# Kernel tuning notes

Hardware: AMD Instinct MI355X
Metric: run time of the kernel (lower is better)

The kernel has to match this reference:

```python
import jax, jax.numpy as jnp
import numpy as np

NHEAD = 8

def setup_inputs() -> dict:
    key = jax.random.key(0)
    ks = jax.random.split(key, 7)
    B, N, D = 8, 1024, 512
    scale = 1.0 / np.sqrt(D)
    return {
        "x": jax.random.normal(ks[0], (B, N, D), dtype=jnp.float32),
        "graph_bias": jax.random.normal(ks[1], (B, N, N), dtype=jnp.float32),
        "in_proj_w": jax.random.normal(ks[2], (3 * D, D), dtype=jnp.float32) * scale,
        "in_proj_b": jax.random.normal(ks[3], (3 * D,), dtype=jnp.float32) * 0.02,
        "out_proj_w": jax.random.normal(ks[4], (D, D), dtype=jnp.float32) * scale,
        "out_proj_b": jax.random.normal(ks[5], (D,), dtype=jnp.float32) * 0.02,
        "bias_strength": jnp.ones((), dtype=jnp.float32),
    }

def reference(x, graph_bias, in_proj_w, in_proj_b, out_proj_w, out_proj_b, bias_strength):
    B, N, D = x.shape
    H = NHEAD
    hd = D // H
    # fused QKV projection (matches nn.MultiheadAttention in_proj)
    qkv = x @ in_proj_w.T + in_proj_b          # (B, N, 3D)
    q, k, v = jnp.split(qkv, 3, axis=-1)
    # (B, H, N, hd)
    q = q.reshape(B, N, H, hd).transpose(0, 2, 1, 3)
    k = k.reshape(B, N, H, hd).transpose(0, 2, 1, 3)
    v = v.reshape(B, N, H, hd).transpose(0, 2, 1, 3)
    # additive bias from predicted causal structure
    alpha = jax.nn.sigmoid(bias_strength)
    causal_mask = jax.nn.sigmoid(graph_bias).transpose(0, 2, 1)   # (B, N, N)
    causal_mask = alpha * causal_mask + (1.0 - alpha) * 0.5
    attn_bias = (causal_mask - 0.5) * 10.0                        # (B, N, N)
    scores = jnp.einsum("bhqd,bhkd->bhqk", q, k) / jnp.sqrt(jnp.asarray(hd, x.dtype))
    scores = scores + attn_bias[:, None, :, :]                    # broadcast over heads
    probs = jax.nn.softmax(scores, axis=-1)
    out = jnp.einsum("bhqk,bhkd->bhqd", probs, v)                 # (B, H, N, hd)
    out = out.transpose(0, 2, 1, 3).reshape(B, N, D)
    return out @ out_proj_w.T + out_proj_b
```

## Files before the change

kernel.cpp:

```cpp
#include <hip/hip_runtime.h>

typedef __attribute__((ext_vector_type(8))) __bf16 bf16x8;
typedef __attribute__((ext_vector_type(4))) __bf16 bf16x4;
typedef __attribute__((ext_vector_type(4))) float f32x4;
typedef __attribute__((ext_vector_type(8))) _Float16 f16x8;

#define LOG2E 1.44269504088896340736f

__device__ __forceinline__ void async_load16(const void* g, void* l) {
  __builtin_amdgcn_global_load_lds(
      (const __attribute__((address_space(1))) void*)g,
      (__attribute__((address_space(3))) void*)l, 16, 0, 0);
}

__device__ __forceinline__ float fast_exp2(float x) {
#if __has_builtin(__builtin_amdgcn_exp2f)
  return __builtin_amdgcn_exp2f(x);
#else
  return __expf(x * 0.6931471805599453f);
#endif
}

__global__ __launch_bounds__(256) void prep(
    const float* __restrict__ gbias, const float* __restrict__ bstr,
    _Float16* __restrict__ ebT,
    const float* __restrict__ a, __bf16* __restrict__ oa, int na4,
    const float* __restrict__ b2, __bf16* __restrict__ ob, int nb4,
    const float* __restrict__ c, __bf16* __restrict__ oc, int nc4) {
  if (blockIdx.x < 4096) {
    const int gid = blockIdx.x * 256 + threadIdx.x;
    const int lane = gid & 63;
    const int kt = (gid >> 6) & 31;
    const int qt = (gid >> 11) & 63;
    const int b = gid >> 17;
    const int g = lane >> 4, ln = lane & 15;
    const float alpha = 1.f / (1.f + __expf(-bstr[0]));
    const float bsc = 10.f * alpha * LOG2E;
    const float* base = gbias + (size_t)(b * 1024 + kt * 32 + ln) * 1024 + qt * 16 + g * 4;
    float4 va = *(const float4*)(base);
    float4 vb = *(const float4*)(base + 16 * 1024);
    float sv[8] = {va.x, va.y, va.z, va.w, vb.x, vb.y, vb.z, vb.w};
    f16x8 o;
#pragma unroll
    for (int i = 0; i < 8; ++i)
      o[i] = (_Float16)((1.f / (1.f + __expf(-sv[i])) - 0.5f) * bsc);
    *(f16x8*)(ebT + (size_t)gid * 8) = o;
  } else {
    int i = (blockIdx.x - 4096) * 256 + threadIdx.x;
    int n = na4 + nb4 + nc4;
    int stride = 2560 * 256;
    for (; i < n; i += stride) {
      const float4* s;
      bf16x4* d;
      int j;
      if (i < na4) { s = (const float4*)a; d = (bf16x4*)oa; j = i; }
      else if (i < na4 + nb4) { s = (const float4*)b2; d = (bf16x4*)ob; j = i - na4; }
      else { s = (const float4*)c; d = (bf16x4*)oc; j = i - na4 - nb4; }
      float4 v = s[j];
      bf16x4 o;
      o[0] = (__bf16)v.x; o[1] = (__bf16)v.y; o[2] = (__bf16)v.z; o[3] = (__bf16)v.w;
      d[j] = o;
    }
  }
}

template <int MODE>
__global__ __launch_bounds__(256) void gemm_bt(
    const __bf16* __restrict__ A, const __bf16* __restrict__ Bm,
    const float* __restrict__ bias, void* __restrict__ C0,
    __bf16* __restrict__ vT, int M, int N, int K) {
  __shared__ __align__(16) char smem[32768];
  char* lA = smem;
  char* lB = smem + 16384;
  const int t = threadIdx.x;
  const int lane = t & 63;
  const int wid = t >> 6;
  const int wm = wid >> 1, wn = wid & 1;
  const int g = lane >> 4, ln = lane & 15;
  const int m0 = blockIdx.y * 128;
  const int n0 = blockIdx.x * 128;

  const int srow = t >> 3;
  const int sswz = ((t & 7) * 16) ^ ((srow & 7) << 4);
  const size_t KB = (size_t)K * 2;
  const char* gA = (const char*)A + (size_t)m0 * KB;
  const char* gB = (const char*)Bm + (size_t)n0 * KB;

  f32x4 acc[4][4] = {};

  for (int k0 = 0; k0 < K; k0 += 64) {
    __syncthreads();
#pragma unroll
    for (int c = 0; c < 4; ++c) {
      int row = srow + 32 * c;
      async_load16(gA + (size_t)row * KB + k0 * 2 + sswz, lA + c * 4096 + t * 16);
      async_load16(gB + (size_t)row * KB + k0 * 2 + sswz, lB + c * 4096 + t * 16);
    }
    __syncthreads();
#pragma unroll
    for (int ks = 0; ks < 2; ++ks) {
      bf16x8 af[4], bf[4];
#pragma unroll
      for (int i = 0; i < 4; ++i) {
        int ar = wm * 64 + i * 16 + ln;
        int byo = (ks * 64 + g * 16) ^ ((ar & 7) << 4);
        af[i] = *(const bf16x8*)(lA + ar * 128 + byo);
        int br = wn * 64 + i * 16 + ln;
        bf[i] = *(const bf16x8*)(lB + br * 128 + byo);
      }
#pragma unroll
      for (int i = 0; i < 4; ++i)
#pragma unroll
        for (int j = 0; j < 4; ++j)
          acc[i][j] = __builtin_amdgcn_mfma_f32_16x16x32_bf16(af[i], bf[j], acc[i][j], 0, 0, 0);
    }
  }

#pragma unroll
  for (int j = 0; j < 4; ++j) {
    int col = n0 + wn * 64 + j * 16 + ln;
    float bv = bias[col];
    if (MODE == 0) {
#pragma unroll
      for (int i = 0; i < 4; ++i) {
        int row0 = m0 + wm * 64 + i * 16 + g * 4;
#pragma unroll
        for (int r = 0; r < 4; ++r)
          ((float*)C0)[(size_t)(row0 + r) * N + col] = acc[i][j][r] + bv;
      }
    } else if (col < 1024) {
      float scale = (col < 512) ? (0.125f * LOG2E) : 1.0f;
#pragma unroll
      for (int i = 0; i < 4; ++i) {
        int row0 = m0 + wm * 64 + i * 16 + g * 4;
#pragma unroll
        for (int r = 0; r < 4; ++r)
          ((__bf16*)C0)[(size_t)(row0 + r) * 1024 + col] = (__bf16)((acc[i][j][r] + bv) * scale);
      }
    } else {
      int h = (col - 1024) >> 6;
      int d = (col - 1024) & 63;
#pragma unroll
      for (int i = 0; i < 4; ++i) {
        int row0 = m0 + wm * 64 + i * 16 + g * 4;
        int b = row0 >> 10;
        bf16x4 pk;
#pragma unroll
        for (int r = 0; r < 4; ++r) pk[r] = (__bf16)(acc[i][j][r] + bv);
        *(bf16x4*)(vT + (((size_t)b * 8 + h) * 64 + d) * 1024 + (row0 & 1023)) = pk;
      }
    }
  }
}

__global__ __launch_bounds__(512, 4) void attn_fused(
    const __bf16* __restrict__ qk,
    const __bf16* __restrict__ vT,
    const _Float16* __restrict__ ebT,
    __bf16* __restrict__ attn) {
  __shared__ __align__(16) char smem[40960];
  const int t = threadIdx.x;
  const int lane = t & 63;
  const int wid = t >> 6;
  const int g = lane >> 4, ln = lane & 15;
  const int wg = ((blockIdx.x & 7) << 6) + (blockIdx.x >> 3);
  const int b = wg >> 6;
  const int rem = wg & 63;
  const int h = rem >> 3;
  const int qg = rem & 7;
  const int qt = qg * 8 + wid;
  const int q0 = qt << 4;

  char* Ps = smem + 32768 + wid * 1024;

  bf16x8 qf[2];
#pragma unroll
  for (int ks = 0; ks < 2; ++ks)
    qf[ks] = *(const bf16x8*)(qk + ((size_t)b * 1024 + q0 + ln) * 1024 +
                              h * 64 + ks * 32 + g * 8);

  float l_acc[4] = {0.f, 0.f, 0.f, 0.f};
  f32x4 o_acc[4] = {};

  const int krow = lane >> 3;
  const int ksrc = ((lane & 7) * 16) ^ (krow << 4);
  const int vrow = lane >> 2;
  const int vsrc = ((lane & 3) * 16) ^ ((vrow & 3) << 4);

  const char* qkb = (const char*)qk + (size_t)b * 1024 * 2048;
  const char* vTb = (const char*)vT + (size_t)(b * 8 + h) * 64 * 2048;
  const _Float16* ebp = ebT + (size_t)((b * 64 + qt) * 32) * 512 + lane * 8;

  auto stage = [&](int p, char* set) {
    if (wid < 4) {
      async_load16(qkb + (size_t)((2 * p) * 32 + wid * 8 + krow) * 2048 + 1024 + h * 128 + ksrc,
                   set + wid * 1024 + lane * 16);
      async_load16(qkb + (size_t)((2 * p + 1) * 32 + wid * 8 + krow) * 2048 + 1024 + h * 128 + ksrc,
                   set + 4096 + wid * 1024 + lane * 16);
    } else {
      int cc = wid - 4;
      async_load16(vTb + (size_t)(cc * 16 + vrow) * 2048 + (size_t)(2 * p) * 64 + vsrc,
                   set + 8192 + cc * 1024 + lane * 16);
      async_load16(vTb + (size_t)(cc * 16 + vrow) * 2048 + (size_t)(2 * p + 1) * 64 + vsrc,
                   set + 12288 + cc * 1024 + lane * 16);
    }
  };

  auto process = [&](const char* Kp, const char* Vp, f16x8 ebv) {
    bf16x8 kf[2][2];
#pragma unroll
    for (int ni = 0; ni < 2; ++ni) {
      int br = ni * 16 + ln;
      int sw = (br & 7) << 4;
#pragma unroll
      for (int ks = 0; ks < 2; ++ks)
        kf[ni][ks] = *(const bf16x8*)(Kp + br * 128 + ((ks * 64 + g * 16) ^ sw));
    }
    bf16x8 vf[4];
#pragma unroll
    for (int di = 0; di < 4; ++di)
      vf[di] = *(const bf16x8*)(Vp + (di * 16 + ln) * 64 + ((g * 16) ^ ((ln & 3) << 4)));

    f32x4 lbf0 = {(float)ebv[0], (float)ebv[1], (float)ebv[2], (float)ebv[3]};
    f32x4 lbf1 = {(float)ebv[4], (float)ebv[5], (float)ebv[6], (float)ebv[7]};
    f32x4 s[2];
    s[0] = __builtin_amdgcn_mfma_f32_16x16x32_bf16(qf[0], kf[0][0], lbf0, 0, 0, 0);
    s[0] = __builtin_amdgcn_mfma_f32_16x16x32_bf16(qf[1], kf[0][1], s[0], 0, 0, 0);
    s[1] = __builtin_amdgcn_mfma_f32_16x16x32_bf16(qf[0], kf[1][0], lbf1, 0, 0, 0);
    s[1] = __builtin_amdgcn_mfma_f32_16x16x32_bf16(qf[1], kf[1][1], s[1], 0, 0, 0);

#pragma unroll
    for (int r = 0; r < 4; ++r) {
      float p0 = fast_exp2(s[0][r]);
      float p1 = fast_exp2(s[1][r]);
      s[0][r] = p0; s[1][r] = p1;
      l_acc[r] += p0 + p1;
    }
#pragma unroll
    for (int ni = 0; ni < 2; ++ni)
#pragma unroll
      for (int r = 0; r < 4; ++r) {
        int q = g * 4 + r;
        *(__bf16*)(Ps + q * 64 + ((ni * 32 + ln * 2) ^ (((q >> 1) & 3) << 4))) =
            (__bf16)s[ni][r];
      }
    bf16x8 pf = *(const bf16x8*)(Ps + ln * 64 + ((g * 16) ^ (((ln >> 1) & 3) << 4)));

#pragma unroll
    for (int di = 0; di < 4; ++di)
      o_acc[di] = __builtin_amdgcn_mfma_f32_16x16x32_bf16(pf, vf[di], o_acc[di], 0, 0, 0);
  };

  stage(0, smem);
  f16x8 eba = *(const f16x8*)(ebp);
  f16x8 ebb = *(const f16x8*)(ebp + 512);
  asm volatile("s_waitcnt vmcnt(0)" ::: "memory");
  __syncthreads();

  for (int p = 0; p < 16; ++p) {
    char* cur = smem + (p & 1) * 16384;
    char* nxt = smem + ((p + 1) & 1) * 16384;
    const int pn = (p + 1) & 15;

    stage(pn, nxt);
    f16x8 eba2 = *(const f16x8*)(ebp + (size_t)(2 * pn) * 512);
    f16x8 ebb2 = *(const f16x8*)(ebp + (size_t)(2 * pn + 1) * 512);
    __builtin_amdgcn_sched_barrier(0);

    process(cur, cur + 8192, eba);
    process(cur + 4096, cur + 12288, ebb);

    asm volatile("s_waitcnt vmcnt(0)" ::: "memory");
    __builtin_amdgcn_sched_barrier(0);
    __syncthreads();
    eba = eba2;
    ebb = ebb2;
  }

#pragma unroll
  for (int r = 0; r < 4; ++r) {
    float rs = l_acc[r];
#pragma unroll
    for (int off = 1; off < 16; off <<= 1)
      rs += __shfl_xor(rs, off, 64);
    float inv = 1.f / rs;
    int q = q0 + g * 4 + r;
#pragma unroll
    for (int di = 0; di < 4; ++di)
      attn[((size_t)b * 1024 + q) * 512 + h * 64 + di * 16 + ln] =
          (__bf16)(o_acc[di][r] * inv);
  }
}

extern "C" void kernel_launch(void* const* d_in, const int* in_sizes, int n_in,
                              void* d_out, int out_size, void* d_ws, size_t ws_size,
                              hipStream_t stream) {
  const float* x     = (const float*)d_in[0];
  const float* gb    = (const float*)d_in[1];
  const float* w_in  = (const float*)d_in[2];
  const float* b_in  = (const float*)d_in[3];
  const float* w_out = (const float*)d_in[4];
  const float* b_out = (const float*)d_in[5];
  const float* bstr  = (const float*)d_in[6];

  char* ws = (char*)d_ws;
  __bf16* qk    = (__bf16*)(ws);
  __bf16* vT    = (__bf16*)(ws + 16777216);
  __bf16* xb    = (__bf16*)(ws + 25165824);
  __bf16* w1    = (__bf16*)(ws + 33554432);
  __bf16* w2    = (__bf16*)(ws + 35127296);
  _Float16* ebT = (_Float16*)(ws + 35651584);
  __bf16* attn_buf = xb;

  prep<<<6656, 256, 0, stream>>>(gb, bstr, ebT,
                                 x, xb, (8 * 1024 * 512) / 4,
                                 w_in, w1, (1536 * 512) / 4,
                                 w_out, w2, (512 * 512) / 4);

  gemm_bt<1><<<dim3(12, 64), 256, 0, stream>>>(xb, w1, b_in, qk, vT, 8192, 1536, 512);
  attn_fused<<<512, 512, 0, stream>>>(qk, vT, ebT, attn_buf);
  gemm_bt<0><<<dim3(4, 64), 256, 0, stream>>>(attn_buf, w2, b_out, d_out, nullptr, 8192, 512, 512);
}
```

Measured before the change: 90.32 us.

## Stage four key tiles per attention iteration and remap GEMM blocks across XCDs

```diff
diff --git a/kernel.cpp b/kernel.cpp
--- a/kernel.cpp
+++ b/kernel.cpp
@@ -68,7 +68,7 @@
 __global__ __launch_bounds__(256) void gemm_bt(
     const __bf16* __restrict__ A, const __bf16* __restrict__ Bm,
     const float* __restrict__ bias, void* __restrict__ C0,
-    __bf16* __restrict__ vT, int M, int N, int K) {
+    __bf16* __restrict__ vT, int M, int N, int K, int nt) {
   __shared__ __align__(16) char smem[32768];
   char* lA = smem;
   char* lB = smem + 16384;
@@ -77,8 +77,10 @@
   const int wid = t >> 6;
   const int wm = wid >> 1, wn = wid & 1;
   const int g = lane >> 4, ln = lane & 15;
-  const int m0 = blockIdx.y * 128;
-  const int n0 = blockIdx.x * 128;
+  const int qchunk = gridDim.x >> 3;
+  const int wg = (blockIdx.x & 7) * qchunk + (blockIdx.x >> 3);
+  const int m0 = (wg / nt) * 128;
+  const int n0 = (wg % nt) * 128;
 
   const int srow = t >> 3;
   const int sswz = ((t & 7) * 16) ^ ((srow & 7) << 4);
@@ -158,7 +160,7 @@
     const __bf16* __restrict__ vT,
     const _Float16* __restrict__ ebT,
     __bf16* __restrict__ attn) {
-  __shared__ __align__(16) char smem[40960];
+  __shared__ __align__(16) char smem[73728];
   const int t = threadIdx.x;
   const int lane = t & 63;
   const int wid = t >> 6;
@@ -171,7 +173,7 @@
   const int qt = qg * 8 + wid;
   const int q0 = qt << 4;
 
-  char* Ps = smem + 32768 + wid * 1024;
+  char* Ps = smem + 65536 + wid * 1024;
 
   bf16x8 qf[2];
 #pragma unroll
@@ -193,16 +195,17 @@
 
   auto stage = [&](int p, char* set) {
     if (wid < 4) {
-      async_load16(qkb + (size_t)((2 * p) * 32 + wid * 8 + krow) * 2048 + 1024 + h * 128 + ksrc,
-                   set + wid * 1024 + lane * 16);
-      async_load16(qkb + (size_t)((2 * p + 1) * 32 + wid * 8 + krow) * 2048 + 1024 + h * 128 + ksrc,
-                   set + 4096 + wid * 1024 + lane * 16);
+#pragma unroll
+      for (int j = 0; j < 4; ++j)
+        async_load16(qkb + (size_t)((4 * p + j) * 32 + wid * 8 + krow) * 2048 +
+                         1024 + h * 128 + ksrc,
+                     set + j * 4096 + wid * 1024 + lane * 16);
     } else {
       int cc = wid - 4;
-      async_load16(vTb + (size_t)(cc * 16 + vrow) * 2048 + (size_t)(2 * p) * 64 + vsrc,
-                   set + 8192 + cc * 1024 + lane * 16);
-      async_load16(vTb + (size_t)(cc * 16 + vrow) * 2048 + (size_t)(2 * p + 1) * 64 + vsrc,
-                   set + 12288 + cc * 1024 + lane * 16);
+#pragma unroll
+      for (int j = 0; j < 4; ++j)
+        async_load16(vTb + (size_t)(cc * 16 + vrow) * 2048 + (size_t)(4 * p + j) * 64 + vsrc,
+                     set + 16384 + j * 4096 + cc * 1024 + lane * 16);
     }
   };
 
@@ -252,29 +255,34 @@
   };
 
   stage(0, smem);
-  f16x8 eba = *(const f16x8*)(ebp);
-  f16x8 ebb = *(const f16x8*)(ebp + 512);
+  f16x8 eb0 = *(const f16x8*)(ebp);
+  f16x8 eb1 = *(const f16x8*)(ebp + 512);
+  f16x8 eb2 = *(const f16x8*)(ebp + 1024);
+  f16x8 eb3 = *(const f16x8*)(ebp + 1536);
   asm volatile("s_waitcnt vmcnt(0)" ::: "memory");
   __syncthreads();
 
-  for (int p = 0; p < 16; ++p) {
-    char* cur = smem + (p & 1) * 16384;
-    char* nxt = smem + ((p + 1) & 1) * 16384;
-    const int pn = (p + 1) & 15;
+  for (int p = 0; p < 8; ++p) {
+    char* cur = smem + (p & 1) * 32768;
+    char* nxt = smem + ((p + 1) & 1) * 32768;
+    const int pn = (p + 1) & 7;
 
     stage(pn, nxt);
-    f16x8 eba2 = *(const f16x8*)(ebp + (size_t)(2 * pn) * 512);
-    f16x8 ebb2 = *(const f16x8*)(ebp + (size_t)(2 * pn + 1) * 512);
+    f16x8 ebn0 = *(const f16x8*)(ebp + (size_t)(4 * pn) * 512);
+    f16x8 ebn1 = *(const f16x8*)(ebp + (size_t)(4 * pn + 1) * 512);
+    f16x8 ebn2 = *(const f16x8*)(ebp + (size_t)(4 * pn + 2) * 512);
+    f16x8 ebn3 = *(const f16x8*)(ebp + (size_t)(4 * pn + 3) * 512);
     __builtin_amdgcn_sched_barrier(0);
 
-    process(cur, cur + 8192, eba);
-    process(cur + 4096, cur + 12288, ebb);
+    process(cur,         cur + 16384, eb0);
+    process(cur + 4096,  cur + 20480, eb1);
+    process(cur + 8192,  cur + 24576, eb2);
+    process(cur + 12288, cur + 28672, eb3);
 
     asm volatile("s_waitcnt vmcnt(0)" ::: "memory");
     __builtin_amdgcn_sched_barrier(0);
     __syncthreads();
-    eba = eba2;
-    ebb = ebb2;
+    eb0 = ebn0; eb1 = ebn1; eb2 = ebn2; eb3 = ebn3;
   }
 
 #pragma unroll
@@ -317,7 +325,7 @@
                                  w_in, w1, (1536 * 512) / 4,
                                  w_out, w2, (512 * 512) / 4);
 
-  gemm_bt<1><<<dim3(12, 64), 256, 0, stream>>>(xb, w1, b_in, qk, vT, 8192, 1536, 512);
+  gemm_bt<1><<<768, 256, 0, stream>>>(xb, w1, b_in, qk, vT, 8192, 1536, 512, 12);
   attn_fused<<<512, 512, 0, stream>>>(qk, vT, ebT, attn_buf);
-  gemm_bt<0><<<dim3(4, 64), 256, 0, stream>>>(attn_buf, w2, b_out, d_out, nullptr, 8192, 512, 512);
-}
+  gemm_bt<0><<<256, 256, 0, stream>>>(attn_buf, w2, b_out, d_out, nullptr, 8192, 512, 512, 4);
+}
```

Result: no change. 89.75 us (-0.6%).
